# Performance work log

Hardware: AMD Instinct MI355X
Metric: run time of the kernel (lower is better)

The kernel has to match this reference:

```python
import jax, jax.numpy as jnp
import numpy as np

N_E = 50000
N_R = 1000
E = 800000
E_HIDDEN = 256
R_HIDDEN = 64
NEG_SLOPE = 0.01  # torch F.leaky_relu default


def segment_softmax(logits, seg, num_segments):
    # numerically stable per-segment softmax over edges
    seg_max = jax.ops.segment_max(logits, seg, num_segments=num_segments)
    seg_max = jnp.where(jnp.isfinite(seg_max), seg_max, 0.0)
    ex = jnp.exp(logits - seg_max[seg])
    denom = jax.ops.segment_sum(ex, seg, num_segments=num_segments)
    return ex / (denom[seg] + 1e-16)


def setup_inputs() -> dict:
    key = jax.random.key(0)
    ks = jax.random.split(key, 9)
    return {
        "x_e": jax.random.normal(ks[0], (N_E, E_HIDDEN), dtype=jnp.float32),
        "x_r": jax.random.normal(ks[1], (N_R, R_HIDDEN), dtype=jnp.float32),
        "edge_index": jax.random.randint(ks[2], (2, E), 0, N_E, dtype=jnp.int64),
        "rel": jax.random.randint(ks[3], (E,), 0, N_R, dtype=jnp.int64),
        "line_graph_index": jax.random.randint(ks[4], (2, E), 0, E, dtype=jnp.int64),
        "line_graph_val": jax.random.uniform(ks[5], (E,), dtype=jnp.float32),
        "a_h_w": jax.random.normal(ks[6], (E_HIDDEN,), dtype=jnp.float32),
        "a_t_w": jax.random.normal(ks[7], (E_HIDDEN,), dtype=jnp.float32),
        "a_r_w": jax.random.normal(ks[8], (R_HIDDEN,), dtype=jnp.float32),
    }


def reference(x_e, x_r, edge_index, rel, line_graph_index, line_graph_val, a_h_w, a_t_w, a_r_w):
    head, tail = edge_index[0], edge_index[1]
    # per-node scalar scores, gathered per edge
    s_e_h = jnp.einsum("nd,d->n", x_e, a_h_w)  # [N_e]
    s_e_t = jnp.einsum("nd,d->n", x_e, a_t_w)  # [N_e]
    s_r = jnp.einsum("rd,d->r", x_r, a_r_w)    # [N_r]
    e_h = s_e_h[head]
    e_t = s_e_t[tail]
    e_r = s_r[rel]

    n_e = x_e.shape[0]
    msg = x_r[rel]  # [E, r_hidden]

    # head branch: segment softmax over head groups, scatter-aggregate x_r[rel]
    alpha_h = segment_softmax(jax.nn.leaky_relu(e_h + e_r, NEG_SLOPE), head, n_e)
    x_e_h = jax.ops.segment_sum(alpha_h[:, None] * msg, head, num_segments=n_e)

    # tail branch: softmax grouped by tail, but spmm still scatters into head rows
    alpha_t = segment_softmax(jax.nn.leaky_relu(e_t + e_r, NEG_SLOPE), tail, n_e)
    x_e_t = jax.ops.segment_sum(alpha_t[:, None] * msg, tail, num_segments=n_e)

    return jnp.concatenate([x_e_h, x_e_t], axis=1)  # [N_e, 2*r_hidden]
```

## Files before the change

kernel.cpp:

```cpp
#include <hip/hip_runtime.h>

static constexpr int kNE = 50000;
static constexpr int kNR = 1000;
static constexpr int kE  = 800000;
static constexpr int kEH = 256;
static constexpr int kRH = 64;
static constexpr float kNeg = 0.01f;

static constexpr int kSegsPerB = 64;
static constexpr int kSegs = 2 * kNE;
static constexpr int kB = (kSegs + kSegsPerB - 1) / kSegsPerB;
static constexpr int kCap = 1536;
static constexpr int kEdgesPerBin = 4096;
static constexpr int kBinBlocks  = (kE + kEdgesPerBin - 1) / kEdgesPerBin;
static constexpr int kNodeBlocks = kNE / 8;
static constexpr int kRelBlocks  = kNR / 8;
static constexpr int kCntPad = 2048;

__device__ __forceinline__ float lrelu(float x){ return x > 0.f ? x : kNeg * x; }

__global__ __launch_bounds__(512) void k_bin_scores(
        const float* __restrict__ xe, const float* __restrict__ ahw,
        const float* __restrict__ atw, const float* __restrict__ xr,
        const float* __restrict__ arw,
        const int* __restrict__ head, const int* __restrict__ tail,
        const int* __restrict__ rel,
        float* __restrict__ s_h, float* __restrict__ s_t, float* __restrict__ s_r,
        int* __restrict__ bucket_fill, unsigned short* __restrict__ records){
    __shared__ int cnt[kCntPad];
    __shared__ int cur[kCntPad];
    __shared__ unsigned int srt[2 * kEdgesPerBin];
    __shared__ int wsum[8];

    int blk = blockIdx.x;
    int tid = threadIdx.x;
    int lane = tid & 63;

    if (blk >= kBinBlocks){
        int sb = blk - kBinBlocks;
        if (sb < kNodeBlocks){
            int node = sb * 8 + (tid >> 6);
            const float4* row = (const float4*)(xe + (size_t)node * kEH);
            float4 xv = row[lane];
            float4 av = ((const float4*)ahw)[lane];
            float4 bv = ((const float4*)atw)[lane];
            float ph = xv.x*av.x + xv.y*av.y + xv.z*av.z + xv.w*av.w;
            float pt = xv.x*bv.x + xv.y*bv.y + xv.z*bv.z + xv.w*bv.w;
            #pragma unroll
            for (int o = 32; o > 0; o >>= 1){
                ph += __shfl_down(ph, o, 64);
                pt += __shfl_down(pt, o, 64);
            }
            if (lane == 0){ s_h[node] = ph; s_t[node] = pt; }
        } else {
            int r = (sb - kNodeBlocks) * 8 + (tid >> 6);
            float p = xr[(size_t)r * kRH + lane] * arw[lane];
            #pragma unroll
            for (int o = 32; o > 0; o >>= 1) p += __shfl_down(p, o, 64);
            if (lane == 0) s_r[r] = p;
        }
        return;
    }

    int e0 = blk * kEdgesPerBin;
    for (int i = tid; i < kCntPad; i += 512) cnt[i] = 0;
    __syncthreads();

    unsigned int recs[16];
    unsigned short rnk[16];
    #pragma unroll
    for (int p = 0; p < 8; ++p){
        int e = e0 + p * 512 + tid;
        unsigned int rh = 0xFFFFFFFFu, rt = 0xFFFFFFFFu;
        unsigned short kh = 0, kt = 0;
        if (e < kE){
            int h = head[e], t = tail[e], r = rel[e];
            rh = ((unsigned int)h << 10) | (unsigned int)r;
            rt = ((unsigned int)(kNE + t) << 10) | (unsigned int)r;
            kh = (unsigned short)atomicAdd(&cnt[rh >> 16], 1);
            kt = (unsigned short)atomicAdd(&cnt[rt >> 16], 1);
        }
        recs[p] = rh; recs[8 + p] = rt;
        rnk[p]  = kh; rnk[8 + p]  = kt;
    }
    __syncthreads();

    int c0 = cnt[4 * tid], c1 = cnt[4 * tid + 1], c2 = cnt[4 * tid + 2], c3 = cnt[4 * tid + 3];
    int v = c0 + c1 + c2 + c3;
    int x = v;
    #pragma unroll
    for (int o = 1; o < 64; o <<= 1){
        int y = __shfl_up(x, o, 64);
        if (lane >= o) x += y;
    }
    int wv = tid >> 6;
    if (lane == 63) wsum[wv] = x;
    __syncthreads();
    int wpre = 0, tot = 0;
    #pragma unroll
    for (int w = 0; w < 8; ++w){
        int s = wsum[w];
        if (w < wv) wpre += s;
        tot += s;
    }
    int base = wpre + x - v;
    cur[4 * tid]     = base;
    cur[4 * tid + 1] = base + c0;
    cur[4 * tid + 2] = base + c0 + c1;
    cur[4 * tid + 3] = base + c0 + c1 + c2;
    __syncthreads();

    #pragma unroll
    for (int p = 0; p < 16; ++p){
        unsigned int rc = recs[p];
        if (rc != 0xFFFFFFFFu){
            int slot = cur[rc >> 16] + (int)rnk[p];
            srt[slot] = rc;
        }
    }
    __syncthreads();

    for (int i = tid; i < kB; i += 512){
        int c = cnt[i];
        if (c > 0){
            int gb = atomicAdd(&bucket_fill[i], c);
            cur[i] = gb - cur[i];
        }
    }
    __syncthreads();

    for (int j = tid; j < tot; j += 512){
        unsigned int rc = srt[j];
        int bk = rc >> 16;
        int g  = cur[bk] + j;
        if (g < kCap) records[(size_t)bk * kCap + g] = (unsigned short)(rc & 0xFFFFu);
    }
}

__global__ __launch_bounds__(256) void k_sort_aggregate(
        const int* __restrict__ bucket_fill, const unsigned short* __restrict__ records,
        const float* __restrict__ s_h, const float* __restrict__ s_t,
        const float* __restrict__ s_r, const float* __restrict__ xr,
        float* __restrict__ out){
    __shared__ float srl[kNR];
    __shared__ float sn[kSegsPerB];
    __shared__ unsigned short relbuf[kCap];
    __shared__ float alphabuf[kCap];
    __shared__ int cnt[kSegsPerB], start[kSegsPerB];
    __shared__ unsigned short order[kSegsPerB];

    int b = blockIdx.x;
    int tid = threadIdx.x;

    for (int i = tid; i < kNR; i += 256) srl[i] = s_r[i];
    if (tid < kSegsPerB){
        cnt[tid] = 0;
        int gseg = b * kSegsPerB + tid;
        float s = 0.f;
        if (gseg < kNE) s = s_h[gseg];
        else if (gseg < kSegs) s = s_t[gseg - kNE];
        sn[tid] = s;
    }
    __syncthreads();

    int nrec = bucket_fill[b];
    if (nrec > kCap) nrec = kCap;
    const unsigned short* rb = records + (size_t)b * kCap;

    unsigned short recs[6], rnk[6];
    #pragma unroll
    for (int p = 0; p < 6; ++p){
        int idx = p * 256 + tid;
        unsigned short rc = 0xFFFFu, rk = 0;
        if (idx < nrec){
            rc = rb[idx];
            rk = (unsigned short)atomicAdd(&cnt[rc >> 10], 1);
        }
        recs[p] = rc; rnk[p] = rk;
    }
    __syncthreads();
    if (tid < kSegsPerB){
        int c = cnt[tid];
        int x = c;
        #pragma unroll
        for (int o = 1; o < 64; o <<= 1){
            int y = __shfl_up(x, o, 64);
            if (tid >= o) x += y;
        }
        start[tid] = x - c;

        unsigned int key = ((unsigned int)c << 6) | (unsigned int)tid;
        #pragma unroll
        for (int k = 2; k <= 64; k <<= 1){
            #pragma unroll
            for (int j = k >> 1; j > 0; j >>= 1){
                unsigned int o2 = __shfl_xor(key, j, 64);
                bool keepMin = (((tid & j) == 0) == ((tid & k) == 0));
                unsigned int mn = key < o2 ? key : o2;
                unsigned int mx = key < o2 ? o2 : key;
                key = keepMin ? mn : mx;
            }
        }
        order[tid] = (unsigned short)(key & 63u);
    }
    __syncthreads();
    #pragma unroll
    for (int p = 0; p < 6; ++p){
        unsigned short rc = recs[p];
        if (rc != 0xFFFFu){
            int ls = rc >> 10;
            int rr = rc & 1023;
            int slot = start[ls] + (int)rnk[p];
            relbuf[slot] = (unsigned short)rr;
            alphabuf[slot] = lrelu(sn[ls] + srl[rr]);
        }
    }
    __syncthreads();

    int grp = tid >> 4;
    int sub = tid & 15;
    #pragma unroll
    for (int i = 0; i < 4; ++i){
        int ls = order[i * 16 + grp];
        int gseg = b * kSegsPerB + ls;
        if (gseg >= kSegs) continue;
        int deg = cnt[ls], st = start[ls];

        float part = -INFINITY;
        for (int k = sub; k < deg; k += 16) part = fmaxf(part, alphabuf[st + k]);
        #pragma unroll
        for (int o = 1; o < 16; o <<= 1) part = fmaxf(part, __shfl_xor(part, o, 64));
        float m = part;

        float ss = 0.f;
        for (int k = sub; k < deg; k += 16){
            float e = __expf(alphabuf[st + k] - m);
            alphabuf[st + k] = e;
            ss += e;
        }
        #pragma unroll
        for (int o = 1; o < 16; o <<= 1) ss += __shfl_xor(ss, o, 64);
        float inv = 1.f / (ss + 1e-16f);

        float4 acc = {0.f, 0.f, 0.f, 0.f};
        int k = 0;
        for (; k + 4 <= deg; k += 4){
            int r0 = relbuf[st + k],     r1 = relbuf[st + k + 1];
            int r2 = relbuf[st + k + 2], r3 = relbuf[st + k + 3];
            float a0 = alphabuf[st + k],     a1 = alphabuf[st + k + 1];
            float a2 = alphabuf[st + k + 2], a3 = alphabuf[st + k + 3];
            float4 v0 = ((const float4*)(xr + (size_t)r0 * kRH))[sub];
            float4 v1 = ((const float4*)(xr + (size_t)r1 * kRH))[sub];
            float4 v2 = ((const float4*)(xr + (size_t)r2 * kRH))[sub];
            float4 v3 = ((const float4*)(xr + (size_t)r3 * kRH))[sub];
            acc.x += a0*v0.x + a1*v1.x + a2*v2.x + a3*v3.x;
            acc.y += a0*v0.y + a1*v1.y + a2*v2.y + a3*v3.y;
            acc.z += a0*v0.z + a1*v1.z + a2*v2.z + a3*v3.z;
            acc.w += a0*v0.w + a1*v1.w + a2*v2.w + a3*v3.w;
        }
        for (; k < deg; ++k){
            int rr = relbuf[st + k];
            float a = alphabuf[st + k];
            float4 v = ((const float4*)(xr + (size_t)rr * kRH))[sub];
            acc.x += a*v.x; acc.y += a*v.y; acc.z += a*v.z; acc.w += a*v.w;
        }
        acc.x *= inv; acc.y *= inv; acc.z *= inv; acc.w *= inv;

        bool isHead = gseg < kNE;
        int node = isHead ? gseg : gseg - kNE;
        float4* op = (float4*)(out + (size_t)node * (2 * kRH) + (isHead ? 0 : kRH));
        op[sub] = acc;
    }
}

extern "C" void kernel_launch(void* const* d_in, const int* in_sizes, int n_in,
                              void* d_out, int out_size, void* d_ws, size_t ws_size,
                              hipStream_t stream) {
    const float* xe  = (const float*)d_in[0];
    const float* xr  = (const float*)d_in[1];
    const int* edge_index = (const int*)d_in[2];
    const int* rel        = (const int*)d_in[3];
    const float* ahw = (const float*)d_in[6];
    const float* atw = (const float*)d_in[7];
    const float* arw = (const float*)d_in[8];
    float* out = (float*)d_out;

    const int* head = edge_index;
    const int* tail = edge_index + kE;

    char* ws = (char*)d_ws;
    float* s_h  = (float*)ws;                    ws += kNE * sizeof(float);
    float* s_t  = (float*)ws;                    ws += kNE * sizeof(float);
    float* s_r  = (float*)ws;                    ws += kNR * sizeof(float);
    int*   bucket_fill = (int*)ws;               ws += ((kB + 255) & ~255) * sizeof(int);
    unsigned short* records = (unsigned short*)ws; ws += (size_t)kB * kCap * sizeof(unsigned short);

    hipMemsetAsync(bucket_fill, 0, kB * sizeof(int), stream);
    k_bin_scores<<<kBinBlocks + kNodeBlocks + kRelBlocks, 512, 0, stream>>>(
        xe, ahw, atw, xr, arw, head, tail, rel, s_h, s_t, s_r, bucket_fill, records);
    k_sort_aggregate<<<kB, 256, 0, stream>>>(bucket_fill, records, s_h, s_t, s_r, xr, out);
}
```

Baseline: 155.9 us.

## Replace global atomic bucket scatter with per-chunk sorted runs and offset table

The binning kernel no longer does global atomicAdd on bucket fill counters and scattered record writes. Each bin block now writes its locally sorted records contiguously to its own chunk and records per-bucket start offsets in a transposed table. The aggregate kernel prefix-sums run lengths across all 391 chunks and gathers its bucket's records into shared memory. The memset is dropped, edges per bin are halved, and the per-segment max is computed with shared atomicMax during the scatter instead of a separate pass. The cost is many small uncoalesced serial reads per thread in the gather loop, plus a 392-column table scan per block.

```diff
diff --git a/kernel.cpp b/kernel.cpp
--- a/kernel.cpp
+++ b/kernel.cpp
@@ -11,8 +11,10 @@
 static constexpr int kSegs = 2 * kNE;
 static constexpr int kB = (kSegs + kSegsPerB - 1) / kSegsPerB;
 static constexpr int kCap = 1536;
-static constexpr int kEdgesPerBin = 4096;
+static constexpr int kEdgesPerBin = 2048;
+static constexpr int kChunkRecs  = 2 * kEdgesPerBin;
 static constexpr int kBinBlocks  = (kE + kEdgesPerBin - 1) / kEdgesPerBin;
+static constexpr int kTabCols    = 392;
 static constexpr int kNodeBlocks = kNE / 8;
 static constexpr int kRelBlocks  = kNR / 8;
 static constexpr int kCntPad = 2048;
@@ -26,10 +28,10 @@
         const int* __restrict__ head, const int* __restrict__ tail,
         const int* __restrict__ rel,
         float* __restrict__ s_h, float* __restrict__ s_t, float* __restrict__ s_r,
-        int* __restrict__ bucket_fill, unsigned short* __restrict__ records){
+        unsigned short* __restrict__ chunk, unsigned short* __restrict__ tab){
     __shared__ int cnt[kCntPad];
     __shared__ int cur[kCntPad];
-    __shared__ unsigned int srt[2 * kEdgesPerBin];
+    __shared__ unsigned int srt[kChunkRecs];
     __shared__ int wsum[8];
 
     int blk = blockIdx.x;
@@ -66,10 +68,10 @@
     for (int i = tid; i < kCntPad; i += 512) cnt[i] = 0;
     __syncthreads();
 
-    unsigned int recs[16];
-    unsigned short rnk[16];
-    #pragma unroll
-    for (int p = 0; p < 8; ++p){
+    unsigned int recs[8];
+    unsigned short rnk[8];
+    #pragma unroll
+    for (int p = 0; p < 4; ++p){
         int e = e0 + p * 512 + tid;
         unsigned int rh = 0xFFFFFFFFu, rt = 0xFFFFFFFFu;
         unsigned short kh = 0, kt = 0;
@@ -80,8 +82,8 @@
             kh = (unsigned short)atomicAdd(&cnt[rh >> 16], 1);
             kt = (unsigned short)atomicAdd(&cnt[rt >> 16], 1);
         }
-        recs[p] = rh; recs[8 + p] = rt;
-        rnk[p]  = kh; rnk[8 + p]  = kt;
+        recs[p] = rh; recs[4 + p] = rt;
+        rnk[p]  = kh; rnk[4 + p]  = kt;
     }
     __syncthreads();
 
@@ -111,7 +113,7 @@
     __syncthreads();
 
     #pragma unroll
-    for (int p = 0; p < 16; ++p){
+    for (int p = 0; p < 8; ++p){
         unsigned int rc = recs[p];
         if (rc != 0xFFFFFFFFu){
             int slot = cur[rc >> 16] + (int)rnk[p];
@@ -120,41 +122,42 @@
     }
     __syncthreads();
 
-    for (int i = tid; i < kB; i += 512){
-        int c = cnt[i];
-        if (c > 0){
-            int gb = atomicAdd(&bucket_fill[i], c);
-            cur[i] = gb - cur[i];
-        }
-    }
-    __syncthreads();
-
-    for (int j = tid; j < tot; j += 512){
-        unsigned int rc = srt[j];
-        int bk = rc >> 16;
-        int g  = cur[bk] + j;
-        if (g < kCap) records[(size_t)bk * kCap + g] = (unsigned short)(rc & 0xFFFFu);
-    }
+    unsigned int* cw = (unsigned int*)(chunk + (size_t)blk * kChunkRecs);
+    for (int j2 = tid; j2 < (tot >> 1); j2 += 512){
+        unsigned int lo = srt[2 * j2] & 0xFFFFu;
+        unsigned int hi = srt[2 * j2 + 1] & 0xFFFFu;
+        cw[j2] = lo | (hi << 16);
+    }
+    for (int i = tid; i < kB; i += 512)
+        tab[(size_t)i * kTabCols + blk] = (unsigned short)cur[i];
+    if (tid == 0)
+        tab[(size_t)kB * kTabCols + blk] = (unsigned short)tot;
 }
 
 __global__ __launch_bounds__(256) void k_sort_aggregate(
-        const int* __restrict__ bucket_fill, const unsigned short* __restrict__ records,
+        const unsigned short* __restrict__ chunk, const unsigned short* __restrict__ tab,
         const float* __restrict__ s_h, const float* __restrict__ s_t,
         const float* __restrict__ s_r, const float* __restrict__ xr,
         float* __restrict__ out){
     __shared__ float srl[kNR];
     __shared__ float sn[kSegsPerB];
+    __shared__ unsigned short arr[kCap];
     __shared__ unsigned short relbuf[kCap];
     __shared__ float alphabuf[kCap];
     __shared__ int cnt[kSegsPerB], start[kSegsPerB];
+    __shared__ unsigned int mx[kSegsPerB];
     __shared__ unsigned short order[kSegsPerB];
+    __shared__ int gsum[4];
 
     int b = blockIdx.x;
     int tid = threadIdx.x;
+    int lane = tid & 63;
+    int wv = tid >> 6;
 
     for (int i = tid; i < kNR; i += 256) srl[i] = s_r[i];
     if (tid < kSegsPerB){
         cnt[tid] = 0;
+        mx[tid] = 0u;
         int gseg = b * kSegsPerB + tid;
         float s = 0.f;
         if (gseg < kNE) s = s_h[gseg];
@@ -163,9 +166,39 @@
     }
     __syncthreads();
 
-    int nrec = bucket_fill[b];
+    const unsigned short* rowS = tab + (size_t)b * kTabCols;
+    const unsigned short* rowE = tab + (size_t)(b + 1) * kTabCols;
+    int nrec = 0;
+    for (int c0 = 0; c0 < kBinBlocks; c0 += 256){
+        int c = c0 + tid;
+        int s = 0, L = 0;
+        if (c < kBinBlocks){
+            s = rowS[c];
+            L = (int)rowE[c] - s;
+        }
+        int x = L;
+        #pragma unroll
+        for (int o = 1; o < 64; o <<= 1){
+            int y = __shfl_up(x, o, 64);
+            if (lane >= o) x += y;
+        }
+        if (lane == 63) gsum[wv] = x;
+        __syncthreads();
+        int wpre = 0, stot = 0;
+        #pragma unroll
+        for (int w = 0; w < 4; ++w){
+            int g = gsum[w];
+            if (w < wv) wpre += g;
+            stot += g;
+        }
+        int off = nrec + wpre + x - L;
+        if (off + L > kCap) L = max(0, kCap - off);
+        const unsigned short* src = chunk + (size_t)c * kChunkRecs + s;
+        for (int i = 0; i < L; ++i) arr[off + i] = src[i];
+        nrec += stot;
+        __syncthreads();
+    }
     if (nrec > kCap) nrec = kCap;
-    const unsigned short* rb = records + (size_t)b * kCap;
 
     unsigned short recs[6], rnk[6];
     #pragma unroll
@@ -173,7 +206,7 @@
         int idx = p * 256 + tid;
         unsigned short rc = 0xFFFFu, rk = 0;
         if (idx < nrec){
-            rc = rb[idx];
+            rc = arr[idx];
             rk = (unsigned short)atomicAdd(&cnt[rc >> 10], 1);
         }
         recs[p] = rc; rnk[p] = rk;
@@ -197,8 +230,8 @@
                 unsigned int o2 = __shfl_xor(key, j, 64);
                 bool keepMin = (((tid & j) == 0) == ((tid & k) == 0));
                 unsigned int mn = key < o2 ? key : o2;
-                unsigned int mx = key < o2 ? o2 : key;
-                key = keepMin ? mn : mx;
+                unsigned int mxk = key < o2 ? o2 : key;
+                key = keepMin ? mn : mxk;
             }
         }
         order[tid] = (unsigned short)(key & 63u);
@@ -211,8 +244,12 @@
             int ls = rc >> 10;
             int rr = rc & 1023;
             int slot = start[ls] + (int)rnk[p];
+            float lg = lrelu(sn[ls] + srl[rr]);
+            unsigned int s32 = __float_as_uint(lg);
+            unsigned int key = (s32 & 0x80000000u) ? ~s32 : (s32 | 0x80000000u);
+            atomicMax(&mx[ls], key);
             relbuf[slot] = (unsigned short)rr;
-            alphabuf[slot] = lrelu(sn[ls] + srl[rr]);
+            alphabuf[slot] = lg;
         }
     }
     __syncthreads();
@@ -226,11 +263,8 @@
         if (gseg >= kSegs) continue;
         int deg = cnt[ls], st = start[ls];
 
-        float part = -INFINITY;
-        for (int k = sub; k < deg; k += 16) part = fmaxf(part, alphabuf[st + k]);
-        #pragma unroll
-        for (int o = 1; o < 16; o <<= 1) part = fmaxf(part, __shfl_xor(part, o, 64));
-        float m = part;
+        unsigned int u = mx[ls];
+        float m = __uint_as_float((u & 0x80000000u) ? (u & 0x7FFFFFFFu) : ~u);
 
         float ss = 0.f;
         for (int k = sub; k < deg; k += 16){
@@ -291,12 +325,11 @@
     char* ws = (char*)d_ws;
     float* s_h  = (float*)ws;                    ws += kNE * sizeof(float);
     float* s_t  = (float*)ws;                    ws += kNE * sizeof(float);
-    float* s_r  = (float*)ws;                    ws += kNR * sizeof(float);
-    int*   bucket_fill = (int*)ws;               ws += ((kB + 255) & ~255) * sizeof(int);
-    unsigned short* records = (unsigned short*)ws; ws += (size_t)kB * kCap * sizeof(unsigned short);
-
-    hipMemsetAsync(bucket_fill, 0, kB * sizeof(int), stream);
+    float* s_r  = (float*)ws;                    ws += ((kNR + 256) & ~255) * sizeof(float);
+    unsigned short* chunk = (unsigned short*)ws; ws += (size_t)kBinBlocks * kChunkRecs * sizeof(unsigned short);
+    unsigned short* tab   = (unsigned short*)ws; ws += (size_t)(kB + 1) * kTabCols * sizeof(unsigned short);
+
     k_bin_scores<<<kBinBlocks + kNodeBlocks + kRelBlocks, 512, 0, stream>>>(
-        xe, ahw, atw, xr, arw, head, tail, rel, s_h, s_t, s_r, bucket_fill, records);
-    k_sort_aggregate<<<kB, 256, 0, stream>>>(bucket_fill, records, s_h, s_t, s_r, xr, out);
+        xe, ahw, atw, xr, arw, head, tail, rel, s_h, s_t, s_r, chunk, tab);
+    k_sort_aggregate<<<kB, 256, 0, stream>>>(chunk, tab, s_h, s_t, s_r, xr, out);
 }
```

After: 149.0 us. -4.4%, faster.
